# Kernel tuning notes

Hardware: AMD Instinct MI355X
Metric: run time of the kernel (lower is better)

Reference implementation:

```python
import jax, jax.numpy as jnp
import numpy as np

B, T, IN, H, OUT = 16384, 32, 64, 512, 19


def setup_inputs() -> dict:
    key = jax.random.key(0)
    ks = jax.random.split(key, 10)
    s = 0.05
    return {
        "input_data": jax.random.normal(ks[0], (B, T, IN), dtype=jnp.float32),
        "Wx0": jax.random.normal(ks[1], (IN, 4 * H), dtype=jnp.float32) * s,
        "Wh0": jax.random.normal(ks[2], (H, 4 * H), dtype=jnp.float32) * s,
        "b0": jnp.zeros((4 * H,), dtype=jnp.float32),
        "Wx1": jax.random.normal(ks[3], (H + 1, 4 * H), dtype=jnp.float32) * s,
        "Wh1": jax.random.normal(ks[4], (H, 4 * H), dtype=jnp.float32) * s,
        "b1": jnp.zeros((4 * H,), dtype=jnp.float32),
        "Wlin": jax.random.normal(ks[5], (H, OUT), dtype=jnp.float32) * s,
        "blin": jnp.zeros((OUT,), dtype=jnp.float32),
        "time_step": T,
    }


def _lstm_gates(x, h, c, Wx, Wh, b):
    # PyTorch LSTMCell gate order: i, f, g, o
    g = x @ Wx + h @ Wh + b
    i, f, gc, o = jnp.split(g, 4, axis=-1)
    cn = jax.nn.sigmoid(f) * c + jax.nn.sigmoid(i) * jnp.tanh(gc)
    hn = jax.nn.sigmoid(o) * jnp.tanh(cn)
    return hn, cn


def reference(input_data, Wx0, Wh0, b0, Wx1, Wh1, b1, Wlin, blin, time_step):
    batch = input_data.shape[0]
    hidden = Wh0.shape[0]

    def step(carry, x_t):
        h0, c0, h1, c1 = carry
        flag = x_t[:, :1]  # condition flag in feature column 0
        # cell 1: condition-gated LSTM update
        h0n, c0n = _lstm_gates(x_t, h0, c0, Wx0, Wh0, b0)
        h0 = flag * h0n + (1.0 - flag) * h0
        c0 = flag * c0n + (1.0 - flag) * c0
        # cell 2 input: [flag, h0]
        x2 = jnp.concatenate([flag, h0], axis=1)
        h1n, c1n = _lstm_gates(x2, h1, c1, Wx1, Wh1, b1)
        h1 = flag * h1n + (1.0 - flag) * h1
        c1 = flag * c1n + (1.0 - flag) * c1
        return (h0, c0, h1, c1), None

    z = jnp.zeros((batch, hidden), dtype=input_data.dtype)
    xs = jnp.swapaxes(input_data[:, :time_step, :], 0, 1)  # [T, B, IN]
    (h0, c0, h1, c1), _ = jax.lax.scan(step, (z, z, z, z), xs)
    return h1 @ Wlin + blin
```

## Files before the change

### kernel.cpp

```cpp
#include <hip/hip_runtime.h>
#include <hip/hip_bf16.h>


#define T_STEPS 32
#define IN_F    64
#define HID     512
#define OUT_F   19
#define BW      64

typedef short bf16x8 __attribute__((ext_vector_type(8)));
typedef float f32x4  __attribute__((ext_vector_type(4)));

__device__ __forceinline__ float fast_sig(float x) {
    return __builtin_amdgcn_rcpf(1.0f + __expf(-x));
}
__device__ __forceinline__ float fast_tanh(float x) {
    return 1.0f - 2.0f * __builtin_amdgcn_rcpf(1.0f + __expf(2.0f * x));
}

#define LBAR() do { \
    asm volatile("s_waitcnt lgkmcnt(0)" ::: "memory"); \
    __builtin_amdgcn_sched_barrier(0); \
    __builtin_amdgcn_s_barrier(); \
    __builtin_amdgcn_sched_barrier(0); \
} while (0)

#define MFMA16(A0, A1, A2, A3, Q0, Q1, Q2, Q3) do { \
    acc[0][0] = __builtin_amdgcn_mfma_f32_16x16x32_bf16(A0, Q0, acc[0][0], 0, 0, 0); \
    acc[1][0] = __builtin_amdgcn_mfma_f32_16x16x32_bf16(A1, Q0, acc[1][0], 0, 0, 0); \
    acc[2][0] = __builtin_amdgcn_mfma_f32_16x16x32_bf16(A2, Q0, acc[2][0], 0, 0, 0); \
    acc[3][0] = __builtin_amdgcn_mfma_f32_16x16x32_bf16(A3, Q0, acc[3][0], 0, 0, 0); \
    acc[0][1] = __builtin_amdgcn_mfma_f32_16x16x32_bf16(A0, Q1, acc[0][1], 0, 0, 0); \
    acc[1][1] = __builtin_amdgcn_mfma_f32_16x16x32_bf16(A1, Q1, acc[1][1], 0, 0, 0); \
    acc[2][1] = __builtin_amdgcn_mfma_f32_16x16x32_bf16(A2, Q1, acc[2][1], 0, 0, 0); \
    acc[3][1] = __builtin_amdgcn_mfma_f32_16x16x32_bf16(A3, Q1, acc[3][1], 0, 0, 0); \
    acc[0][2] = __builtin_amdgcn_mfma_f32_16x16x32_bf16(A0, Q2, acc[0][2], 0, 0, 0); \
    acc[1][2] = __builtin_amdgcn_mfma_f32_16x16x32_bf16(A1, Q2, acc[1][2], 0, 0, 0); \
    acc[2][2] = __builtin_amdgcn_mfma_f32_16x16x32_bf16(A2, Q2, acc[2][2], 0, 0, 0); \
    acc[3][2] = __builtin_amdgcn_mfma_f32_16x16x32_bf16(A3, Q2, acc[3][2], 0, 0, 0); \
    acc[0][3] = __builtin_amdgcn_mfma_f32_16x16x32_bf16(A0, Q3, acc[0][3], 0, 0, 0); \
    acc[1][3] = __builtin_amdgcn_mfma_f32_16x16x32_bf16(A1, Q3, acc[1][3], 0, 0, 0); \
    acc[2][3] = __builtin_amdgcn_mfma_f32_16x16x32_bf16(A2, Q3, acc[2][3], 0, 0, 0); \
    acc[3][3] = __builtin_amdgcn_mfma_f32_16x16x32_bf16(A3, Q3, acc[3][3], 0, 0, 0); \
} while (0)

__global__ void wprep_kernel(const float* __restrict__ src,
                             __hip_bfloat16* __restrict__ dst,
                             int kcBits, int rowOff) {
    int idx = blockIdx.x * 256 + threadIdx.x;
    int total = 2048 << (kcBits + 5);
    if (idx >= total) return;
    int e   = idx & 7;
    int lq  = (idx >> 3) & 3;
    int l15 = (idx >> 5) & 15;
    int kc  = (idx >> 9) & ((1 << kcBits) - 1);
    int cb  = idx >> (9 + kcBits);
    int k   = kc * 32 + lq * 8 + e + rowOff;
    int col = cb * 16 + l15;
    dst[idx] = __float2bfloat16(src[(size_t)k * 2048 + col]);
}

template<int KC, int RTS>
__device__ __forceinline__ void gemm_sec4(const char* aE, const char* aO,
                                          const __hip_bfloat16* b0p,
                                          const __hip_bfloat16* b1p,
                                          const __hip_bfloat16* b2p,
                                          const __hip_bfloat16* b3p,
                                          f32x4 acc[4][4]) {
    bf16x8 pa0, pa1, pa2, pa3, pb0, pb1, pb2, pb3, a0, a1, a2, a3;
    pa0 = *(const bf16x8*)(b0p);
    pa1 = *(const bf16x8*)(b1p);
    pa2 = *(const bf16x8*)(b2p);
    pa3 = *(const bf16x8*)(b3p);
    #pragma unroll 1
    for (int m = 0; m < KC - 2; m += 2) {
        const int ao = (m >> 1) * 128;
        pb0 = *(const bf16x8*)(b0p + (m + 1) * 512);
        pb1 = *(const bf16x8*)(b1p + (m + 1) * 512);
        pb2 = *(const bf16x8*)(b2p + (m + 1) * 512);
        pb3 = *(const bf16x8*)(b3p + (m + 1) * 512);
        a0 = *(const bf16x8*)(aE + ao);
        a1 = *(const bf16x8*)(aE + RTS + ao);
        a2 = *(const bf16x8*)(aE + 2 * RTS + ao);
        a3 = *(const bf16x8*)(aE + 3 * RTS + ao);
        MFMA16(a0, a1, a2, a3, pa0, pa1, pa2, pa3);
        pa0 = *(const bf16x8*)(b0p + (m + 2) * 512);
        pa1 = *(const bf16x8*)(b1p + (m + 2) * 512);
        pa2 = *(const bf16x8*)(b2p + (m + 2) * 512);
        pa3 = *(const bf16x8*)(b3p + (m + 2) * 512);
        a0 = *(const bf16x8*)(aO + ao);
        a1 = *(const bf16x8*)(aO + RTS + ao);
        a2 = *(const bf16x8*)(aO + 2 * RTS + ao);
        a3 = *(const bf16x8*)(aO + 3 * RTS + ao);
        MFMA16(a0, a1, a2, a3, pb0, pb1, pb2, pb3);
    }
    {
        const int ao = ((KC - 2) >> 1) * 128;
        pb0 = *(const bf16x8*)(b0p + (KC - 1) * 512);
        pb1 = *(const bf16x8*)(b1p + (KC - 1) * 512);
        pb2 = *(const bf16x8*)(b2p + (KC - 1) * 512);
        pb3 = *(const bf16x8*)(b3p + (KC - 1) * 512);
        a0 = *(const bf16x8*)(aE + ao);
        a1 = *(const bf16x8*)(aE + RTS + ao);
        a2 = *(const bf16x8*)(aE + 2 * RTS + ao);
        a3 = *(const bf16x8*)(aE + 3 * RTS + ao);
        MFMA16(a0, a1, a2, a3, pa0, pa1, pa2, pa3);
        a0 = *(const bf16x8*)(aO + ao);
        a1 = *(const bf16x8*)(aO + RTS + ao);
        a2 = *(const bf16x8*)(aO + 2 * RTS + ao);
        a3 = *(const bf16x8*)(aO + 3 * RTS + ao);
        MFMA16(a0, a1, a2, a3, pb0, pb1, pb2, pb3);
    }
}

__global__ __launch_bounds__(512, 2)
void lstm_main(const float* __restrict__ x,
               const float* __restrict__ b0v,
               const float* __restrict__ Wx1,
               const float* __restrict__ b1v,
               const float* __restrict__ Wlin,
               const float* __restrict__ blin,
               const __hip_bfloat16* __restrict__ Wx0p,
               const __hip_bfloat16* __restrict__ Wh0p,
               const __hip_bfloat16* __restrict__ Wx1hp,
               const __hip_bfloat16* __restrict__ Wh1p,
               float* __restrict__ cws,
               float* __restrict__ hws,
               float* __restrict__ out)
{
    __shared__ __align__(16) __hip_bfloat16 h0s[BW * HID];
    __shared__ __align__(16) __hip_bfloat16 h1s[BW * HID];
    __shared__ __align__(16) __hip_bfloat16 xs[BW * IN_F];
    __shared__ float flags0[BW];
    __shared__ float flags1[BW];

    const int tid  = threadIdx.x;
    const int lane = tid & 63;
    const int wid  = tid >> 6;
    const int l15  = lane & 15;
    const int lq   = lane >> 4;
    const int lq16 = lq * 16;
    const int laneoff = l15 * 32 + lq * 8;
    const int asw  = (l15 & 7) << 4;
    const int wg   = blockIdx.x;
    const size_t bbase = (size_t)wg * BW;
    const char* xsC = (const char*)xs;
    const char* h0C = (const char*)h0s;
    const int stag = (wid >> 2) * 2;

    const int swE = lq16 ^ asw;
    const int swO = (64 + lq16) ^ asw;
    const char* ahE = h0C + l15 * 1024 + swE;
    const char* ahO = h0C + l15 * 1024 + swO;
    const int h1d = (int)((const char*)h1s - (const char*)h0s);
    const char* axE = xsC + l15 * 128 + swE;
    const char* axO = xsC + l15 * 128 + swO;

    const size_t wsWG0 = (size_t)(0 * 256 + wg) * 32768;
    const size_t wsWG1 = (size_t)(1 * 256 + wg) * 32768;

    auto do_L1 = [&](bool zstate) {
        #pragma unroll 1
        for (int sbi = 0; sbi < 4; ++sbi) {
            const int b2 = ((sbi + stag) & 3) * 8 + wid;
            f32x4 acc[4][4];
            { f32x4 zz = {0.f, 0.f, 0.f, 0.f};
              #pragma unroll
              for (int rt = 0; rt < 4; ++rt)
                  #pragma unroll
                  for (int g = 0; g < 4; ++g) acc[rt][g] = zz; }

            gemm_sec4<16, 16384>(ahE, ahO,
                Wx1hp + (size_t)(0 * 32 + b2) * 8192 + laneoff,
                Wx1hp + (size_t)(1 * 32 + b2) * 8192 + laneoff,
                Wx1hp + (size_t)(2 * 32 + b2) * 8192 + laneoff,
                Wx1hp + (size_t)(3 * 32 + b2) * 8192 + laneoff, acc);
            gemm_sec4<16, 16384>(ahE + h1d, ahO + h1d,
                Wh1p + (size_t)(0 * 32 + b2) * 8192 + laneoff,
                Wh1p + (size_t)(1 * 32 + b2) * 8192 + laneoff,
                Wh1p + (size_t)(2 * 32 + b2) * 8192 + laneoff,
                Wh1p + (size_t)(3 * 32 + b2) * 8192 + laneoff, acc);

            const size_t sbase = wsWG1 + (size_t)b2 * 1024 + lane * 4;
            f32x4 cold[4], hold[4];
            if (!zstate) {
                #pragma unroll
                for (int rt = 0; rt < 4; ++rt) {
                    cold[rt] = __builtin_nontemporal_load((const f32x4*)(cws + sbase + rt * 256));
                    hold[rt] = *(const f32x4*)(hws + sbase + rt * 256);
                }
            } else {
                f32x4 zz = {0.f, 0.f, 0.f, 0.f};
                #pragma unroll
                for (int rt = 0; rt < 4; ++rt) { cold[rt] = zz; hold[rt] = zz; }
            }
            const int jcol = b2 * 16 + l15;
            float bia[4], w10[4];
            #pragma unroll
            for (int g = 0; g < 4; ++g) {
                bia[g] = b1v[g * 512 + jcol];
                w10[g] = Wx1[g * 512 + jcol];
            }
            #pragma unroll
            for (int rt = 0; rt < 4; ++rt) {
                f32x4 cnew, hnew;
                #pragma unroll
                for (int r = 0; r < 4; ++r) {
                    const float f = flags0[rt * 16 + lq * 4 + r];
                    float gi = acc[rt][0][r] + bia[0] + f * w10[0];
                    float gf = acc[rt][1][r] + bia[1] + f * w10[1];
                    float gg = acc[rt][2][r] + bia[2] + f * w10[2];
                    float go = acc[rt][3][r] + bia[3] + f * w10[3];
                    float cn = fast_sig(gf) * cold[rt][r] + fast_sig(gi) * fast_tanh(gg);
                    float hn = fast_sig(go) * fast_tanh(cn);
                    cnew[r] = f * cn + (1.f - f) * cold[rt][r];
                    hnew[r] = f * hn + (1.f - f) * hold[rt][r];
                }
                __builtin_nontemporal_store(cnew, (f32x4*)(cws + sbase + rt * 256));
                *(f32x4*)(hws + sbase + rt * 256) = hnew;
            }
        }
    };

    auto do_L0 = [&](bool zstate) {
        #pragma unroll 1
        for (int sbi = 0; sbi < 4; ++sbi) {
            const int b2 = ((sbi + stag) & 3) * 8 + wid;
            f32x4 acc[4][4];
            { f32x4 zz = {0.f, 0.f, 0.f, 0.f};
              #pragma unroll
              for (int rt = 0; rt < 4; ++rt)
                  #pragma unroll
                  for (int g = 0; g < 4; ++g) acc[rt][g] = zz; }

            {
                const __hip_bfloat16* bx0 = Wx0p + (size_t)(0 * 32 + b2) * 1024 + laneoff;
                const __hip_bfloat16* bx1 = Wx0p + (size_t)(1 * 32 + b2) * 1024 + laneoff;
                const __hip_bfloat16* bx2 = Wx0p + (size_t)(2 * 32 + b2) * 1024 + laneoff;
                const __hip_bfloat16* bx3 = Wx0p + (size_t)(3 * 32 + b2) * 1024 + laneoff;
                bf16x8 pa0 = *(const bf16x8*)(bx0);
                bf16x8 pa1 = *(const bf16x8*)(bx1);
                bf16x8 pa2 = *(const bf16x8*)(bx2);
                bf16x8 pa3 = *(const bf16x8*)(bx3);
                bf16x8 pb0 = *(const bf16x8*)(bx0 + 512);
                bf16x8 pb1 = *(const bf16x8*)(bx1 + 512);
                bf16x8 pb2 = *(const bf16x8*)(bx2 + 512);
                bf16x8 pb3 = *(const bf16x8*)(bx3 + 512);
                bf16x8 a0 = *(const bf16x8*)(axE);
                bf16x8 a1 = *(const bf16x8*)(axE + 2048);
                bf16x8 a2 = *(const bf16x8*)(axE + 4096);
                bf16x8 a3 = *(const bf16x8*)(axE + 6144);
                MFMA16(a0, a1, a2, a3, pa0, pa1, pa2, pa3);
                a0 = *(const bf16x8*)(axO);
                a1 = *(const bf16x8*)(axO + 2048);
                a2 = *(const bf16x8*)(axO + 4096);
                a3 = *(const bf16x8*)(axO + 6144);
                MFMA16(a0, a1, a2, a3, pb0, pb1, pb2, pb3);
            }
            gemm_sec4<16, 16384>(ahE, ahO,
                Wh0p + (size_t)(0 * 32 + b2) * 8192 + laneoff,
                Wh0p + (size_t)(1 * 32 + b2) * 8192 + laneoff,
                Wh0p + (size_t)(2 * 32 + b2) * 8192 + laneoff,
                Wh0p + (size_t)(3 * 32 + b2) * 8192 + laneoff, acc);

            const size_t sbase = wsWG0 + (size_t)b2 * 1024 + lane * 4;
            f32x4 cold[4], hold[4];
            if (!zstate) {
                #pragma unroll
                for (int rt = 0; rt < 4; ++rt) {
                    cold[rt] = __builtin_nontemporal_load((const f32x4*)(cws + sbase + rt * 256));
                    hold[rt] = *(const f32x4*)(hws + sbase + rt * 256);
                }
            } else {
                f32x4 zz = {0.f, 0.f, 0.f, 0.f};
                #pragma unroll
                for (int rt = 0; rt < 4; ++rt) { cold[rt] = zz; hold[rt] = zz; }
            }
            const int jcol = b2 * 16 + l15;
            float bia[4];
            #pragma unroll
            for (int g = 0; g < 4; ++g) bia[g] = b0v[g * 512 + jcol];
            #pragma unroll
            for (int rt = 0; rt < 4; ++rt) {
                f32x4 cnew, hnew;
                #pragma unroll
                for (int r = 0; r < 4; ++r) {
                    const float f = flags1[rt * 16 + lq * 4 + r];
                    float gi = acc[rt][0][r] + bia[0];
                    float gf = acc[rt][1][r] + bia[1];
                    float gg = acc[rt][2][r] + bia[2];
                    float go = acc[rt][3][r] + bia[3];
                    float cn = fast_sig(gf) * cold[rt][r] + fast_sig(gi) * fast_tanh(gg);
                    float hn = fast_sig(go) * fast_tanh(cn);
                    cnew[r] = f * cn + (1.f - f) * cold[rt][r];
                    hnew[r] = f * hn + (1.f - f) * hold[rt][r];
                }
                __builtin_nontemporal_store(cnew, (f32x4*)(cws + sbase + rt * 256));
                *(f32x4*)(hws + sbase + rt * 256) = hnew;
            }
        }
    };

    auto refill = [&](__hip_bfloat16* dst, size_t wsWG) {
        for (int i4 = tid; i4 < BW * HID / 4; i4 += 512) {
            f32x4 v = *(const f32x4*)(hws + wsWG + (size_t)i4 * 4);
            int lane2 = i4 & 63, rt2 = (i4 >> 6) & 3, b2r = i4 >> 8;
            int col2 = 2 * (b2r * 16 + (lane2 & 15));
            int rowb = rt2 * 16 + (lane2 >> 4) * 4;
            #pragma unroll
            for (int r = 0; r < 4; ++r) {
                int row = rowb + r;
                int byte = row * 1024 + (col2 ^ ((row & 7) << 4));
                *(__hip_bfloat16*)((char*)dst + byte) = __float2bfloat16(v[r]);
            }
        }
    };

    auto stage_x = [&](int tt) {
        for (int i = tid; i < BW * IN_F; i += 512) {
            int row = i >> 6, k = i & 63;
            float v = __builtin_nontemporal_load(&x[(bbase + row) * (T_STEPS * IN_F) + tt * IN_F + k]);
            int byte = row * 128 + ((2 * k) ^ ((row & 7) << 4));
            *(__hip_bfloat16*)((char*)xs + byte) = __float2bfloat16(v);
        }
    };

    {
        int4 z; z.x = z.y = z.z = z.w = 0;
        int4* p0 = (int4*)h0s; int4* p1 = (int4*)h1s;
        for (int i = tid; i < BW * HID * 2 / 16; i += 512) { p0[i] = z; p1[i] = z; }
    }
    stage_x(0);
    if (tid < BW) {
        float f0 = x[(bbase + tid) * (T_STEPS * IN_F)];
        flags0[tid] = f0;
        flags1[tid] = f0;
    }
    LBAR();

    do_L0(true);
    __syncthreads();
    refill(h0s, wsWG0);
    stage_x(1);
    if (tid < BW) flags1[tid] = x[(bbase + tid) * (T_STEPS * IN_F) + IN_F];
    LBAR();

    #pragma unroll 1
    for (int t = 0; t < T_STEPS - 1; ++t) {
        do_L1(t == 0);
        do_L0(false);
        __syncthreads();
        refill(h0s, wsWG0);
        refill(h1s, wsWG1);
        if (tid < BW) {
            float f1 = flags1[tid];
            flags0[tid] = f1;
            flags1[tid] = (t + 2 < T_STEPS)
                ? x[(bbase + tid) * (T_STEPS * IN_F) + (size_t)(t + 2) * IN_F] : 0.f;
        }
        if (t + 2 < T_STEPS) stage_x(t + 2);
        LBAR();
    }

    do_L1(false);
    __syncthreads();

    for (int task = tid; task < BW * OUT_F; task += 512) {
        int o   = task >> 6;
        int row = task & 63;
        const int base_row = ((row >> 4) << 8) + (((row >> 2) & 3) << 6) + (row & 3);
        float s = blin[o];
        const float* hp = hws + wsWG1 + base_row;
        const float* wl = Wlin + o;
        #pragma unroll 1
        for (int kb = 0; kb < 32; ++kb) {
            #pragma unroll
            for (int kl = 0; kl < 16; ++kl)
                s += hp[kb * 1024 + kl * 4] * wl[(kb * 16 + kl) * OUT_F];
        }
        out[(bbase + row) * OUT_F + o] = s;
    }
}

extern "C" void kernel_launch(void* const* d_in, const int* in_sizes, int n_in,
                              void* d_out, int out_size, void* d_ws, size_t ws_size,
                              hipStream_t stream) {
    const float* x    = (const float*)d_in[0];
    const float* Wx0  = (const float*)d_in[1];
    const float* Wh0  = (const float*)d_in[2];
    const float* b0   = (const float*)d_in[3];
    const float* Wx1  = (const float*)d_in[4];
    const float* Wh1  = (const float*)d_in[5];
    const float* b1   = (const float*)d_in[6];
    const float* Wlin = (const float*)d_in[7];
    const float* blin = (const float*)d_in[8];

    const size_t offWx0p  = 0;
    const size_t offWh0p  = 262144;
    const size_t offWx1hp = 2359296;
    const size_t offWh1p  = 4456448;
    const size_t offC     = 6553600;
    const size_t offH     = 73662464;
    const size_t needed   = 140771328;
    if (ws_size < needed) return;

    char* w = (char*)d_ws;
    __hip_bfloat16* Wx0p  = (__hip_bfloat16*)(w + offWx0p);
    __hip_bfloat16* Wh0p  = (__hip_bfloat16*)(w + offWh0p);
    __hip_bfloat16* Wx1hp = (__hip_bfloat16*)(w + offWx1hp);
    __hip_bfloat16* Wh1p  = (__hip_bfloat16*)(w + offWh1p);
    float* cws = (float*)(w + offC);
    float* hws = (float*)(w + offH);

    dim3 blk(256);
    wprep_kernel<<<(2048 * 64 + 255) / 256, blk, 0, stream>>>(Wx0, Wx0p, 1, 0);
    wprep_kernel<<<(2048 * 512 + 255) / 256, blk, 0, stream>>>(Wh0, Wh0p, 4, 0);
    wprep_kernel<<<(2048 * 512 + 255) / 256, blk, 0, stream>>>(Wx1, Wx1hp, 4, 1);
    wprep_kernel<<<(2048 * 512 + 255) / 256, blk, 0, stream>>>(Wh1, Wh1p, 4, 0);

    lstm_main<<<256, 512, 0, stream>>>(x, b0, Wx1, b1, Wlin, blin,
                                       Wx0p, Wh0p, Wx1hp, Wh1p, cws, hws, (float*)d_out);
}
```

Baseline: 5.100 ms.

## Halve batch tile per workgroup to 32 rows and launch 512 workgroups

Shrinks the per-workgroup batch tile from 64 to 32 rows and doubles the grid to 512 workgroups. The MFMA inner blocks drop from 4 to 2 row tiles, and the workspace indexing, refill and output projection are rescaled to match. This spreads the work over more CUs (MI355X has 256) and cuts per-wave register and LDS use. In exchange, each bf16 weight fragment loaded from global or L2 is reused across half as many rows, roughly doubling total weight traffic. It also removes the per-wave staggering of column-block order.

```diff
diff --git a/kernel.cpp b/kernel.cpp
--- a/kernel.cpp
+++ b/kernel.cpp
@@ -6,7 +6,8 @@
 #define IN_F    64
 #define HID     512
 #define OUT_F   19
-#define BW      64
+#define BW      32
+#define NWG     512
 
 typedef short bf16x8 __attribute__((ext_vector_type(8)));
 typedef float f32x4  __attribute__((ext_vector_type(4)));
@@ -25,23 +26,15 @@
     __builtin_amdgcn_sched_barrier(0); \
 } while (0)
 
-#define MFMA16(A0, A1, A2, A3, Q0, Q1, Q2, Q3) do { \
+#define MFMA8(A0, A1, Q0, Q1, Q2, Q3) do { \
     acc[0][0] = __builtin_amdgcn_mfma_f32_16x16x32_bf16(A0, Q0, acc[0][0], 0, 0, 0); \
     acc[1][0] = __builtin_amdgcn_mfma_f32_16x16x32_bf16(A1, Q0, acc[1][0], 0, 0, 0); \
-    acc[2][0] = __builtin_amdgcn_mfma_f32_16x16x32_bf16(A2, Q0, acc[2][0], 0, 0, 0); \
-    acc[3][0] = __builtin_amdgcn_mfma_f32_16x16x32_bf16(A3, Q0, acc[3][0], 0, 0, 0); \
     acc[0][1] = __builtin_amdgcn_mfma_f32_16x16x32_bf16(A0, Q1, acc[0][1], 0, 0, 0); \
     acc[1][1] = __builtin_amdgcn_mfma_f32_16x16x32_bf16(A1, Q1, acc[1][1], 0, 0, 0); \
-    acc[2][1] = __builtin_amdgcn_mfma_f32_16x16x32_bf16(A2, Q1, acc[2][1], 0, 0, 0); \
-    acc[3][1] = __builtin_amdgcn_mfma_f32_16x16x32_bf16(A3, Q1, acc[3][1], 0, 0, 0); \
     acc[0][2] = __builtin_amdgcn_mfma_f32_16x16x32_bf16(A0, Q2, acc[0][2], 0, 0, 0); \
     acc[1][2] = __builtin_amdgcn_mfma_f32_16x16x32_bf16(A1, Q2, acc[1][2], 0, 0, 0); \
-    acc[2][2] = __builtin_amdgcn_mfma_f32_16x16x32_bf16(A2, Q2, acc[2][2], 0, 0, 0); \
-    acc[3][2] = __builtin_amdgcn_mfma_f32_16x16x32_bf16(A3, Q2, acc[3][2], 0, 0, 0); \
     acc[0][3] = __builtin_amdgcn_mfma_f32_16x16x32_bf16(A0, Q3, acc[0][3], 0, 0, 0); \
     acc[1][3] = __builtin_amdgcn_mfma_f32_16x16x32_bf16(A1, Q3, acc[1][3], 0, 0, 0); \
-    acc[2][3] = __builtin_amdgcn_mfma_f32_16x16x32_bf16(A2, Q3, acc[2][3], 0, 0, 0); \
-    acc[3][3] = __builtin_amdgcn_mfma_f32_16x16x32_bf16(A3, Q3, acc[3][3], 0, 0, 0); \
 } while (0)
 
 __global__ void wprep_kernel(const float* __restrict__ src,
@@ -61,13 +54,13 @@
 }
 
 template<int KC, int RTS>
-__device__ __forceinline__ void gemm_sec4(const char* aE, const char* aO,
+__device__ __forceinline__ void gemm_sec2(const char* aE, const char* aO,
                                           const __hip_bfloat16* b0p,
                                           const __hip_bfloat16* b1p,
                                           const __hip_bfloat16* b2p,
                                           const __hip_bfloat16* b3p,
-                                          f32x4 acc[4][4]) {
-    bf16x8 pa0, pa1, pa2, pa3, pb0, pb1, pb2, pb3, a0, a1, a2, a3;
+                                          f32x4 acc[2][4]) {
+    bf16x8 pa0, pa1, pa2, pa3, pb0, pb1, pb2, pb3, a0, a1;
     pa0 = *(const bf16x8*)(b0p);
     pa1 = *(const bf16x8*)(b1p);
     pa2 = *(const bf16x8*)(b2p);
@@ -81,18 +74,14 @@
         pb3 = *(const bf16x8*)(b3p + (m + 1) * 512);
         a0 = *(const bf16x8*)(aE + ao);
         a1 = *(const bf16x8*)(aE + RTS + ao);
-        a2 = *(const bf16x8*)(aE + 2 * RTS + ao);
-        a3 = *(const bf16x8*)(aE + 3 * RTS + ao);
-        MFMA16(a0, a1, a2, a3, pa0, pa1, pa2, pa3);
+        MFMA8(a0, a1, pa0, pa1, pa2, pa3);
         pa0 = *(const bf16x8*)(b0p + (m + 2) * 512);
         pa1 = *(const bf16x8*)(b1p + (m + 2) * 512);
         pa2 = *(const bf16x8*)(b2p + (m + 2) * 512);
         pa3 = *(const bf16x8*)(b3p + (m + 2) * 512);
         a0 = *(const bf16x8*)(aO + ao);
         a1 = *(const bf16x8*)(aO + RTS + ao);
-        a2 = *(const bf16x8*)(aO + 2 * RTS + ao);
-        a3 = *(const bf16x8*)(aO + 3 * RTS + ao);
-        MFMA16(a0, a1, a2, a3, pb0, pb1, pb2, pb3);
+        MFMA8(a0, a1, pb0, pb1, pb2, pb3);
     }
     {
         const int ao = ((KC - 2) >> 1) * 128;
@@ -102,14 +91,10 @@
         pb3 = *(const bf16x8*)(b3p + (KC - 1) * 512);
         a0 = *(const bf16x8*)(aE + ao);
         a1 = *(const bf16x8*)(aE + RTS + ao);
-        a2 = *(const bf16x8*)(aE + 2 * RTS + ao);
-        a3 = *(const bf16x8*)(aE + 3 * RTS + ao);
-        MFMA16(a0, a1, a2, a3, pa0, pa1, pa2, pa3);
+        MFMA8(a0, a1, pa0, pa1, pa2, pa3);
         a0 = *(const bf16x8*)(aO + ao);
         a1 = *(const bf16x8*)(aO + RTS + ao);
-        a2 = *(const bf16x8*)(aO + 2 * RTS + ao);
-        a3 = *(const bf16x8*)(aO + 3 * RTS + ao);
-        MFMA16(a0, a1, a2, a3, pb0, pb1, pb2, pb3);
+        MFMA8(a0, a1, pb0, pb1, pb2, pb3);
     }
 }
 
@@ -146,7 +131,6 @@
     const size_t bbase = (size_t)wg * BW;
     const char* xsC = (const char*)xs;
     const char* h0C = (const char*)h0s;
-    const int stag = (wid >> 2) * 2;
 
     const int swE = lq16 ^ asw;
     const int swO = (64 + lq16) ^ asw;
@@ -156,43 +140,42 @@
     const char* axE = xsC + l15 * 128 + swE;
     const char* axO = xsC + l15 * 128 + swO;
 
-    const size_t wsWG0 = (size_t)(0 * 256 + wg) * 32768;
-    const size_t wsWG1 = (size_t)(1 * 256 + wg) * 32768;
+    const size_t wsWG0 = (size_t)(0 * NWG + wg) * 16384;
+    const size_t wsWG1 = (size_t)(1 * NWG + wg) * 16384;
 
     auto do_L1 = [&](bool zstate) {
         #pragma unroll 1
-        for (int sbi = 0; sbi < 4; ++sbi) {
-            const int b2 = ((sbi + stag) & 3) * 8 + wid;
-            f32x4 acc[4][4];
+        for (int sb = 0; sb < 4; ++sb) {
+            const int b2 = sb * 8 + wid;
+            f32x4 acc[2][4];
             { f32x4 zz = {0.f, 0.f, 0.f, 0.f};
               #pragma unroll
-              for (int rt = 0; rt < 4; ++rt)
+              for (int rt = 0; rt < 2; ++rt)
                   #pragma unroll
                   for (int g = 0; g < 4; ++g) acc[rt][g] = zz; }
 
-            gemm_sec4<16, 16384>(ahE, ahO,
+            gemm_sec2<16, 16384>(ahE, ahO,
                 Wx1hp + (size_t)(0 * 32 + b2) * 8192 + laneoff,
                 Wx1hp + (size_t)(1 * 32 + b2) * 8192 + laneoff,
                 Wx1hp + (size_t)(2 * 32 + b2) * 8192 + laneoff,
                 Wx1hp + (size_t)(3 * 32 + b2) * 8192 + laneoff, acc);
-            gemm_sec4<16, 16384>(ahE + h1d, ahO + h1d,
+            gemm_sec2<16, 16384>(ahE + h1d, ahO + h1d,
                 Wh1p + (size_t)(0 * 32 + b2) * 8192 + laneoff,
                 Wh1p + (size_t)(1 * 32 + b2) * 8192 + laneoff,
                 Wh1p + (size_t)(2 * 32 + b2) * 8192 + laneoff,
                 Wh1p + (size_t)(3 * 32 + b2) * 8192 + laneoff, acc);
 
-            const size_t sbase = wsWG1 + (size_t)b2 * 1024 + lane * 4;
-            f32x4 cold[4], hold[4];
+            const size_t sbase = wsWG1 + (size_t)b2 * 512 + lane * 4;
+            f32x4 cold[2], hold[2];
             if (!zstate) {
                 #pragma unroll
-                for (int rt = 0; rt < 4; ++rt) {
+                for (int rt = 0; rt < 2; ++rt) {
                     cold[rt] = __builtin_nontemporal_load((const f32x4*)(cws + sbase + rt * 256));
                     hold[rt] = *(const f32x4*)(hws + sbase + rt * 256);
                 }
             } else {
                 f32x4 zz = {0.f, 0.f, 0.f, 0.f};
-                #pragma unroll
-                for (int rt = 0; rt < 4; ++rt) { cold[rt] = zz; hold[rt] = zz; }
+                cold[0] = zz; cold[1] = zz; hold[0] = zz; hold[1] = zz;
             }
             const int jcol = b2 * 16 + l15;
             float bia[4], w10[4];
@@ -202,7 +185,7 @@
                 w10[g] = Wx1[g * 512 + jcol];
             }
             #pragma unroll
-            for (int rt = 0; rt < 4; ++rt) {
+            for (int rt = 0; rt < 2; ++rt) {
                 f32x4 cnew, hnew;
                 #pragma unroll
                 for (int r = 0; r < 4; ++r) {
@@ -224,12 +207,12 @@
 
     auto do_L0 = [&](bool zstate) {
         #pragma unroll 1
-        for (int sbi = 0; sbi < 4; ++sbi) {
-            const int b2 = ((sbi + stag) & 3) * 8 + wid;
-            f32x4 acc[4][4];
+        for (int sb = 0; sb < 4; ++sb) {
+            const int b2 = sb * 8 + wid;
+            f32x4 acc[2][4];
             { f32x4 zz = {0.f, 0.f, 0.f, 0.f};
               #pragma unroll
-              for (int rt = 0; rt < 4; ++rt)
+              for (int rt = 0; rt < 2; ++rt)
                   #pragma unroll
                   for (int g = 0; g < 4; ++g) acc[rt][g] = zz; }
 
@@ -248,40 +231,35 @@
                 bf16x8 pb3 = *(const bf16x8*)(bx3 + 512);
                 bf16x8 a0 = *(const bf16x8*)(axE);
                 bf16x8 a1 = *(const bf16x8*)(axE + 2048);
-                bf16x8 a2 = *(const bf16x8*)(axE + 4096);
-                bf16x8 a3 = *(const bf16x8*)(axE + 6144);
-                MFMA16(a0, a1, a2, a3, pa0, pa1, pa2, pa3);
+                MFMA8(a0, a1, pa0, pa1, pa2, pa3);
                 a0 = *(const bf16x8*)(axO);
                 a1 = *(const bf16x8*)(axO + 2048);
-                a2 = *(const bf16x8*)(axO + 4096);
-                a3 = *(const bf16x8*)(axO + 6144);
-                MFMA16(a0, a1, a2, a3, pb0, pb1, pb2, pb3);
-            }
-            gemm_sec4<16, 16384>(ahE, ahO,
+                MFMA8(a0, a1, pb0, pb1, pb2, pb3);
+            }
+            gemm_sec2<16, 16384>(ahE, ahO,
                 Wh0p + (size_t)(0 * 32 + b2) * 8192 + laneoff,
                 Wh0p + (size_t)(1 * 32 + b2) * 8192 + laneoff,
                 Wh0p + (size_t)(2 * 32 + b2) * 8192 + laneoff,
                 Wh0p + (size_t)(3 * 32 + b2) * 8192 + laneoff, acc);
 
-            const size_t sbase = wsWG0 + (size_t)b2 * 1024 + lane * 4;
-            f32x4 cold[4], hold[4];
+            const size_t sbase = wsWG0 + (size_t)b2 * 512 + lane * 4;
+            f32x4 cold[2], hold[2];
             if (!zstate) {
                 #pragma unroll
-                for (int rt = 0; rt < 4; ++rt) {
+                for (int rt = 0; rt < 2; ++rt) {
                     cold[rt] = __builtin_nontemporal_load((const f32x4*)(cws + sbase + rt * 256));
                     hold[rt] = *(const f32x4*)(hws + sbase + rt * 256);
                 }
             } else {
                 f32x4 zz = {0.f, 0.f, 0.f, 0.f};
-                #pragma unroll
-                for (int rt = 0; rt < 4; ++rt) { cold[rt] = zz; hold[rt] = zz; }
+                cold[0] = zz; cold[1] = zz; hold[0] = zz; hold[1] = zz;
             }
             const int jcol = b2 * 16 + l15;
             float bia[4];
             #pragma unroll
             for (int g = 0; g < 4; ++g) bia[g] = b0v[g * 512 + jcol];
             #pragma unroll
-            for (int rt = 0; rt < 4; ++rt) {
+            for (int rt = 0; rt < 2; ++rt) {
                 f32x4 cnew, hnew;
                 #pragma unroll
                 for (int r = 0; r < 4; ++r) {
@@ -304,7 +282,7 @@
     auto refill = [&](__hip_bfloat16* dst, size_t wsWG) {
         for (int i4 = tid; i4 < BW * HID / 4; i4 += 512) {
             f32x4 v = *(const f32x4*)(hws + wsWG + (size_t)i4 * 4);
-            int lane2 = i4 & 63, rt2 = (i4 >> 6) & 3, b2r = i4 >> 8;
+            int lane2 = i4 & 63, rt2 = (i4 >> 6) & 1, b2r = i4 >> 7;
             int col2 = 2 * (b2r * 16 + (lane2 & 15));
             int rowb = rt2 * 16 + (lane2 >> 4) * 4;
             #pragma unroll
@@ -366,9 +344,9 @@
     __syncthreads();
 
     for (int task = tid; task < BW * OUT_F; task += 512) {
-        int o   = task >> 6;
-        int row = task & 63;
-        const int base_row = ((row >> 4) << 8) + (((row >> 2) & 3) << 6) + (row & 3);
+        int o   = task >> 5;
+        int row = task & 31;
+        const int base_row = (((row >> 4) & 1) << 8) + (((row >> 2) & 3) << 6) + (row & 3);
         float s = blin[o];
         const float* hp = hws + wsWG1 + base_row;
         const float* wl = Wlin + o;
@@ -376,7 +354,7 @@
         for (int kb = 0; kb < 32; ++kb) {
             #pragma unroll
             for (int kl = 0; kl < 16; ++kl)
-                s += hp[kb * 1024 + kl * 4] * wl[(kb * 16 + kl) * OUT_F];
+                s += hp[kb * 512 + kl * 4] * wl[(kb * 16 + kl) * OUT_F];
         }
         out[(bbase + row) * OUT_F + o] = s;
     }
@@ -418,6 +396,6 @@
     wprep_kernel<<<(2048 * 512 + 255) / 256, blk, 0, stream>>>(Wx1, Wx1hp, 4, 1);
     wprep_kernel<<<(2048 * 512 + 255) / 256, blk, 0, stream>>>(Wh1, Wh1p, 4, 0);
 
-    lstm_main<<<256, 512, 0, stream>>>(x, b0, Wx1, b1, Wlin, blin,
+    lstm_main<<<NWG, 512, 0, stream>>>(x, b0, Wx1, b1, Wlin, blin,
                                        Wx0p, Wh0p, Wx1hp, Wh1p, cws, hws, (float*)d_out);
 }
```

After: 7.214 ms. 41.4% more time.
